# Kernel tuning notes

Hardware: AMD Instinct MI355X
Metric: run time of the kernel (lower is better)

## Reference

```python
import jax, jax.numpy as jnp
import numpy as np

D_MODEL = 1024
H = 16
D_K = D_MODEL // H


def setup_inputs() -> dict:
    key = jax.random.key(0)
    ks = jax.random.split(key, 8)
    B, S = 4, 2048
    q = jax.random.normal(ks[0], (B, S, D_MODEL), dtype=jnp.float32)
    k = jax.random.normal(ks[1], (B, S, D_MODEL), dtype=jnp.float32)
    v = jax.random.normal(ks[2], (B, S, D_MODEL), dtype=jnp.float32)
    scale = 1.0 / np.sqrt(D_MODEL)
    W_q = jax.random.normal(ks[3], (H, D_MODEL, D_K), dtype=jnp.float32) * scale
    W_k = jax.random.normal(ks[4], (H, D_MODEL, D_K), dtype=jnp.float32) * scale
    W_v = jax.random.normal(ks[5], (H, D_MODEL, D_K), dtype=jnp.float32) * scale
    W_o = jax.random.normal(ks[6], (D_MODEL, H * D_K), dtype=jnp.float32) * scale
    b_o = jax.random.normal(ks[7], (D_MODEL,), dtype=jnp.float32) * 0.01
    return {"q": q, "k": k, "v": v, "W_q": W_q, "W_k": W_k, "W_v": W_v, "W_o": W_o, "b_o": b_o}


def reference(q, k, v, W_q, W_k, W_v, W_o, b_o):
    # Per-head projections: [B,S,D] x [H,D,dk] -> [H,B,S,dk]
    qh = jnp.einsum('bsd,hdk->hbsk', q, W_q)
    kh = jnp.einsum('bsd,hdk->hbsk', k, W_k)
    vh = jnp.einsum('bsd,hdk->hbsk', v, W_v)
    # Scaled dot-product attention (full score matrix, as in original)
    scores = jnp.einsum('hbsk,hbtk->hbst', qh, kh) / jnp.sqrt(jnp.asarray(D_K, qh.dtype))
    attn = jax.nn.softmax(scores, axis=-1)
    out = jnp.einsum('hbst,hbtk->hbsk', attn, vh)  # [H,B,S,dk]
    # torch.cat(chunks along head dim, dim=2): head-major feature concat -> [B,S,H*dk]
    out = jnp.transpose(out, (1, 2, 0, 3)).reshape(q.shape[0], q.shape[1], H * D_K)
    return out @ W_o.T + b_o
```

## Files before the change

kernel.cpp:

```cpp
#include <hip/hip_runtime.h>

#define S_LEN 2048

typedef __attribute__((ext_vector_type(8))) short v8s;
typedef __attribute__((ext_vector_type(4))) short v4s;
typedef __attribute__((ext_vector_type(4))) float f32x4;
typedef __attribute__((ext_vector_type(4))) unsigned short v4us;
typedef __attribute__((ext_vector_type(4))) unsigned int v4u;

static __device__ __forceinline__ unsigned short f2bf(float x){
  unsigned u = __builtin_bit_cast(unsigned, x);
  u = (u + 0x7fffu + ((u >> 16) & 1u)) >> 16;
  return (unsigned short)u;
}

static __device__ __forceinline__ unsigned pk2(float a, float b){
  unsigned ua = __builtin_bit_cast(unsigned, a) + 0x8000u;
  unsigned ub = __builtin_bit_cast(unsigned, b) + 0x8000u;
  return __builtin_amdgcn_perm(ub, ua, 0x07060302u);
}

static __device__ __forceinline__ void gload16(const void* g, void* l){
  __builtin_amdgcn_global_load_lds((const __attribute__((address_space(1))) void*)g,
                                   (__attribute__((address_space(3))) void*)l, 16, 0, 0);
}

static __device__ __forceinline__ unsigned lds_off(const void* p){
  return (unsigned)(unsigned long long)(__attribute__((address_space(3))) const void*)p;
}

__global__ void conv_w(const float* __restrict__ Wq, const float* __restrict__ Wk,
                       const float* __restrict__ Wv, const float* __restrict__ Wo,
                       unsigned short* __restrict__ outW){
  int i = blockIdx.x*256 + threadIdx.x;
  const int stride = gridDim.x*256;
  for(; i < 4*1048576; i += stride){
    if (i < 3*1048576){
      int which = i >> 20;
      int rem = i & 1048575;
      const float* W = which==0 ? Wq : (which==1 ? Wk : Wv);
      float v = W[rem];
      if (which == 0) v *= 0.18033688011112042f;
      int h = rem >> 16, d = (rem >> 6) & 1023, kk = rem & 63;
      outW[(which<<20) + (((h<<6)+kk)<<10) + d] = f2bf(v);
    } else {
      outW[i] = f2bf(Wo[i - 3*1048576]);
    }
  }
}

__global__ __launch_bounds__(256,2) void gemm_proj(
    const float* __restrict__ Aq, const float* __restrict__ Ak, const float* __restrict__ Avv,
    const unsigned short* __restrict__ Wtb,
    unsigned short* __restrict__ C0, unsigned short* __restrict__ C1, unsigned short* __restrict__ C2){
  __shared__ unsigned short Als[128*64];
  __shared__ unsigned short Bls[128*64];
  const int tid = threadIdx.x;
  const int l = tid & 63, w = tid >> 6;
  const int z = blockIdx.z;
  const float* Af = (z==0) ? Aq : ((z==1) ? Ak : Avv);
  unsigned short* Cb = (z==0) ? C0 : ((z==1) ? C1 : C2);
  int lid = blockIdx.y*8 + blockIdx.x;
  int nid = (lid & 7)*64 + (lid >> 3);
  const int tx = nid & 7, ty = nid >> 3;
  const int m0 = ty*128, n0 = tx*128;
  const int wr = w >> 1, wc = w & 1;

  f32x4 zero = {0.f,0.f,0.f,0.f};
  f32x4 acc[4][4];
  #pragma unroll
  for(int i=0;i<4;i++){
    #pragma unroll
    for(int j=0;j<4;j++) acc[i][j] = zero;
  }

  const int xorm = (l&7)<<4;
  const int g8 = (l>>4)<<3;
  const int rsub = l>>3, csub = l&7;
  const float* Abase = Af + m0*1024;
  const unsigned short* Bbase = Wtb + z*1048576 + n0*1024;

  float4 ar[8];
  #pragma unroll
  for(int i=0;i<4;i++){
    int c = w*4+i, r = c*8+rsub;
    const float4* src = (const float4*)(Abase + r*1024 + csub*8);
    ar[2*i] = src[0]; ar[2*i+1] = src[1];
  }

  for(int kt=0; kt<16; ++kt){
    const int k0 = kt*64;
    #pragma unroll
    for(int i=0;i<4;i++){
      int c = w*4+i, r = c*8+rsub;
      v4u o = { pk2(ar[2*i].x, ar[2*i].y), pk2(ar[2*i].z, ar[2*i].w),
                pk2(ar[2*i+1].x, ar[2*i+1].y), pk2(ar[2*i+1].z, ar[2*i+1].w) };
      *(v4u*)&Als[c*512 + rsub*64 + ((csub ^ (r&7))<<3)] = o;
    }
    #pragma unroll
    for(int i=0;i<4;i++){
      int c = w*4+i, r = c*8+rsub, col = csub ^ (r&7);
      gload16(Bbase + r*1024 + k0 + col*8, (void*)&Bls[c*512]);
    }
    if (kt < 15){
      #pragma unroll
      for(int i=0;i<4;i++){
        int c = w*4+i, r = c*8+rsub;
        const float4* src = (const float4*)(Abase + r*1024 + (k0+64) + csub*8);
        ar[2*i] = src[0]; ar[2*i+1] = src[1];
      }
    }
    __syncthreads();
    const char* Ab = (const char*)Als;
    const char* Bb = (const char*)Bls;
    #pragma unroll
    for(int kk=0; kk<2; ++kk){
      v8s af[4], bfr[4];
      #pragma unroll
      for(int mf=0; mf<4; ++mf){
        int rb = (wr*64 + mf*16 + (l&15))*128;
        v4s lo = *(const v4s*)(Ab + rb + ((kk*64 + g8) ^ xorm));
        v4s hi = *(const v4s*)(Ab + rb + ((kk*64 + 32 + g8) ^ xorm));
        af[mf] = __builtin_shufflevector(lo, hi, 0,1,2,3,4,5,6,7);
      }
      #pragma unroll
      for(int nf=0; nf<4; ++nf){
        int rb = (wc*64 + nf*16 + (l&15))*128;
        v4s lo = *(const v4s*)(Bb + rb + ((kk*64 + g8) ^ xorm));
        v4s hi = *(const v4s*)(Bb + rb + ((kk*64 + 32 + g8) ^ xorm));
        bfr[nf] = __builtin_shufflevector(lo, hi, 0,1,2,3,4,5,6,7);
      }
      #pragma unroll
      for(int mf=0; mf<4; ++mf){
        #pragma unroll
        for(int nf=0; nf<4; ++nf)
          acc[mf][nf] = __builtin_amdgcn_mfma_f32_16x16x32_bf16(af[mf], bfr[nf], acc[mf][nf], 0,0,0);
      }
    }
    __syncthreads();
  }

  const int g4 = (l>>4)<<2;
  #pragma unroll
  for(int mf=0; mf<4; ++mf){
    int rowb = m0 + wr*64 + mf*16 + g4;
    #pragma unroll
    for(int nf=0; nf<4; ++nf){
      int col = n0 + wc*64 + nf*16 + (l&15);
      #pragma unroll
      for(int r=0;r<4;++r)
        Cb[(rowb+r)*1024 + col] = f2bf(acc[mf][nf][r]);
    }
  }
}

template<int EPI>
__global__ __launch_bounds__(256,2) void gemm_bt(const unsigned short* __restrict__ A,
                                                 const unsigned short* __restrict__ Bt,
                                                 void* __restrict__ Cout,
                                                 const float* __restrict__ bias){
  __shared__ unsigned short Als[128*64];
  __shared__ unsigned short Bls[128*64];
  const int tid = threadIdx.x;
  const int l = tid & 63, w = tid >> 6;
  int lid = blockIdx.y*8 + blockIdx.x;
  int nid = (lid & 7)*64 + (lid >> 3);
  const int tx = nid & 7, ty = nid >> 3;
  const int m0 = ty*128, n0 = tx*128;
  const int wr = w >> 1, wc = w & 1;

  f32x4 zero = {0.f,0.f,0.f,0.f};
  f32x4 acc[4][4];
  #pragma unroll
  for(int i=0;i<4;i++){
    #pragma unroll
    for(int j=0;j<4;j++) acc[i][j] = zero;
  }

  const int xorm = (l&7)<<4;
  const int g8 = (l>>4)<<3;
  const int rsub = l>>3, csub = l&7;
  const unsigned short* Abase = A + m0*1024;
  const unsigned short* Bbase = Bt + n0*1024;

  for(int kt=0; kt<16; ++kt){
    const int k0 = kt*64;
    #pragma unroll
    for(int i=0;i<4;i++){
      int c = w*4+i, r = c*8+rsub, col = csub ^ (r&7);
      gload16(Abase + r*1024 + k0 + col*8, (void*)&Als[c*512]);
    }
    #pragma unroll
    for(int i=0;i<4;i++){
      int c = w*4+i, r = c*8+rsub, col = csub ^ (r&7);
      gload16(Bbase + r*1024 + k0 + col*8, (void*)&Bls[c*512]);
    }
    __syncthreads();
    const char* Ab = (const char*)Als;
    const char* Bb = (const char*)Bls;
    #pragma unroll
    for(int kk=0; kk<2; ++kk){
      v8s af[4], bfr[4];
      #pragma unroll
      for(int mf=0; mf<4; ++mf){
        int rb = (wr*64 + mf*16 + (l&15))*128;
        v4s lo = *(const v4s*)(Ab + rb + ((kk*64 + g8) ^ xorm));
        v4s hi = *(const v4s*)(Ab + rb + ((kk*64 + 32 + g8) ^ xorm));
        af[mf] = __builtin_shufflevector(lo, hi, 0,1,2,3,4,5,6,7);
      }
      #pragma unroll
      for(int nf=0; nf<4; ++nf){
        int rb = (wc*64 + nf*16 + (l&15))*128;
        v4s lo = *(const v4s*)(Bb + rb + ((kk*64 + g8) ^ xorm));
        v4s hi = *(const v4s*)(Bb + rb + ((kk*64 + 32 + g8) ^ xorm));
        bfr[nf] = __builtin_shufflevector(lo, hi, 0,1,2,3,4,5,6,7);
      }
      #pragma unroll
      for(int mf=0; mf<4; ++mf){
        #pragma unroll
        for(int nf=0; nf<4; ++nf)
          acc[mf][nf] = __builtin_amdgcn_mfma_f32_16x16x32_bf16(af[mf], bfr[nf], acc[mf][nf], 0,0,0);
      }
    }
    __syncthreads();
  }

  const int g4 = (l>>4)<<2;
  if (EPI == 0){
    unsigned short* C = (unsigned short*)Cout;
    #pragma unroll
    for(int mf=0; mf<4; ++mf){
      int rowb = m0 + wr*64 + mf*16 + g4;
      #pragma unroll
      for(int nf=0; nf<4; ++nf){
        int col = n0 + wc*64 + nf*16 + (l&15);
        #pragma unroll
        for(int r=0;r<4;++r)
          C[(rowb+r)*1024 + col] = f2bf(acc[mf][nf][r]);
      }
    }
  } else {
    float* C = (float*)Cout;
    #pragma unroll
    for(int mf=0; mf<4; ++mf){
      int rowb = m0 + wr*64 + mf*16 + g4;
      #pragma unroll
      for(int nf=0; nf<4; ++nf){
        int col = n0 + wc*64 + nf*16 + (l&15);
        float bv = bias[col];
        #pragma unroll
        for(int r=0;r<4;++r)
          C[(rowb+r)*1024 + col] = acc[mf][nf][r] + bv;
      }
    }
  }
}

__global__ __launch_bounds__(256,2) void attn_fwd(const unsigned short* __restrict__ Q,
                                                  const unsigned short* __restrict__ K,
                                                  const unsigned short* __restrict__ V,
                                                  unsigned short* __restrict__ O){
  __shared__ unsigned short KVls[2][2][64*64];
  const int tid = threadIdx.x;
  const int l = tid & 63, w = tid >> 6;
  int lid = blockIdx.y*16 + blockIdx.x;
  int nid = (lid & 7)*128 + (lid >> 3);
  const int qb = nid & 15, bh = nid >> 4;
  const int b = bh >> 4, h = bh & 15;
  const int base = b*S_LEN*1024 + h*64;
  const int q0 = qb*128;
  const int xorm = (l&7)<<4, g8 = (l>>4)<<3, g4 = (l>>4)<<2;
  const int rsub = l>>3, csub = l&7;

  auto stage_kv = [&](int kt2, int buf){
    const int k0 = kt2*64;
    #pragma unroll
    for(int i=0;i<2;i++){
      int c = w*2+i, r = c*8+rsub, col = csub ^ (r&7);
      gload16(K + base + (k0+r)*1024 + col*8, (void*)&KVls[buf][0][c*512]);
    }
    #pragma unroll
    for(int i=0;i<2;i++){
      int c = w*2+i;
      int e0 = c*512 + l*8;
      int kg = e0>>10, dg = (e0>>8)&3, kin = (e0>>4)&15, din = e0&15;
      gload16(V + base + (k0 + kg*16 + kin)*1024 + dg*16 + din, (void*)&KVls[buf][1][c*512]);
    }
  };

  #pragma unroll
  for(int i=0;i<4;i++){
    int c = w*4+i, r = c*8+rsub, col = csub ^ (r&7);
    gload16(Q + base + (q0+r)*1024 + col*8, (void*)&KVls[1][0][c*512]);
  }
  stage_kv(0, 0);
  __syncthreads();

  v8s qf[2][2];
  {
    const char* Qb = (const char*)&KVls[1][0][0];
    #pragma unroll
    for(int qh=0; qh<2; ++qh){
      int rb = (w*32 + qh*16 + (l&15))*128;
      #pragma unroll
      for(int t=0;t<2;t++){
        v4s lo = *(const v4s*)(Qb + rb + ((t*64 + g8) ^ xorm));
        v4s hi = *(const v4s*)(Qb + rb + ((t*64 + 32 + g8) ^ xorm));
        qf[qh][t] = __builtin_shufflevector(lo, hi, 0,1,2,3,4,5,6,7);
      }
    }
  }
  __builtin_amdgcn_sched_barrier(0);
  __syncthreads();

  f32x4 zero = {0.f,0.f,0.f,0.f};
  f32x4 oacc[2][4];
  #pragma unroll
  for(int qh=0;qh<2;qh++){
    #pragma unroll
    for(int nf=0;nf<4;nf++) oacc[qh][nf] = zero;
  }
  float lsum[2] = {0.f, 0.f};
  const unsigned vbase0 = lds_off(&KVls[0][1][0]) + l*8;
  const unsigned vbase1 = lds_off(&KVls[1][1][0]) + l*8;

  int cur = 0;
  for(int kt=0; kt<32; ++kt){
    if (kt < 31) stage_kv(kt+1, cur^1);

    const char* Kb = (const char*)&KVls[cur][0][0];
    f32x4 sf[2][4];
    #pragma unroll
    for(int mf=0;mf<4;mf++){
      int rb = (mf*16 + (l&15))*128;
      v8s kf[2];
      #pragma unroll
      for(int t=0;t<2;t++){
        v4s lo = *(const v4s*)(Kb + rb + ((t*64 + g8) ^ xorm));
        v4s hi = *(const v4s*)(Kb + rb + ((t*64 + 32 + g8) ^ xorm));
        kf[t] = __builtin_shufflevector(lo, hi, 0,1,2,3,4,5,6,7);
      }
      #pragma unroll
      for(int qh=0;qh<2;qh++){
        sf[qh][mf] = __builtin_amdgcn_mfma_f32_16x16x32_bf16(kf[0], qf[qh][0], zero, 0,0,0);
        sf[qh][mf] = __builtin_amdgcn_mfma_f32_16x16x32_bf16(kf[1], qf[qh][1], sf[qh][mf], 0,0,0);
      }
    }

    const unsigned vb_sel = cur ? vbase1 : vbase0;
    v4s vtr[2][2][4];
    #define TRR(T,H,N,OFF) asm volatile("ds_read_b64_tr_b16 %0, %1 offset:" #OFF \
                     : "=v"(vtr[T][H][N]) : "v"(vb_sel) : "memory")
    TRR(0,0,0,0);    TRR(0,0,1,512);  TRR(0,0,2,1024); TRR(0,0,3,1536);
    TRR(0,1,0,2048); TRR(0,1,1,2560); TRR(0,1,2,3072); TRR(0,1,3,3584);
    TRR(1,0,0,4096); TRR(1,0,1,4608); TRR(1,0,2,5120); TRR(1,0,3,5632);
    TRR(1,1,0,6144); TRR(1,1,1,6656); TRR(1,1,2,7168); TRR(1,1,3,7680);
    #undef TRR

    v8s pa[2][2];
    #pragma unroll
    for(int qh=0;qh<2;qh++){
      unsigned pd[2][4];
      float ls = 0.f;
      #pragma unroll
      for(int mf=0;mf<4;mf++){
        float e0 = __builtin_amdgcn_exp2f(sf[qh][mf][0]);
        float e1 = __builtin_amdgcn_exp2f(sf[qh][mf][1]);
        float e2 = __builtin_amdgcn_exp2f(sf[qh][mf][2]);
        float e3 = __builtin_amdgcn_exp2f(sf[qh][mf][3]);
        ls += (e0+e1)+(e2+e3);
        int t = mf>>1, hf = mf&1;
        pd[t][hf*2+0] = pk2(e0, e1);
        pd[t][hf*2+1] = pk2(e2, e3);
      }
      lsum[qh] += ls;
      #pragma unroll
      for(int t=0;t<2;t++){
        v4u u = { pd[t][0], pd[t][1], pd[t][2], pd[t][3] };
        pa[qh][t] = __builtin_bit_cast(v8s, u);
      }
    }

    asm volatile("s_waitcnt lgkmcnt(0)" ::: "memory");
    __builtin_amdgcn_sched_barrier(0);
    __builtin_amdgcn_s_setprio(1);
    #pragma unroll
    for(int t=0;t<2;t++){
      #pragma unroll
      for(int nf=0;nf<4;nf++){
        v8s vb = __builtin_shufflevector(vtr[t][0][nf], vtr[t][1][nf], 0,1,2,3,4,5,6,7);
        #pragma unroll
        for(int qh=0;qh<2;qh++)
          oacc[qh][nf] = __builtin_amdgcn_mfma_f32_16x16x32_bf16(pa[qh][t], vb, oacc[qh][nf], 0,0,0);
      }
    }
    __builtin_amdgcn_s_setprio(0);
    __syncthreads();
    cur ^= 1;
  }

  #pragma unroll
  for(int qh=0;qh<2;qh++){
    float s = lsum[qh];
    s += __shfl_xor(s, 16, 64);
    s += __shfl_xor(s, 32, 64);
    float i0 = 1.f/__shfl(s, g4+0, 64);
    float i1 = 1.f/__shfl(s, g4+1, 64);
    float i2 = 1.f/__shfl(s, g4+2, 64);
    float i3 = 1.f/__shfl(s, g4+3, 64);
    const int row = q0 + w*32 + qh*16 + g4;
    #pragma unroll
    for(int nf=0;nf<4;nf++){
      int col = nf*16 + (l&15);
      O[base + (row+0)*1024 + col] = f2bf(oacc[qh][nf][0]*i0);
      O[base + (row+1)*1024 + col] = f2bf(oacc[qh][nf][1]*i1);
      O[base + (row+2)*1024 + col] = f2bf(oacc[qh][nf][2]*i2);
      O[base + (row+3)*1024 + col] = f2bf(oacc[qh][nf][3]*i3);
    }
  }
}

extern "C" void kernel_launch(void* const* d_in, const int* in_sizes, int n_in,
                              void* d_out, int out_size, void* d_ws, size_t ws_size,
                              hipStream_t stream) {
  (void)in_sizes; (void)n_in; (void)out_size;
  const float* q  = (const float*)d_in[0];
  const float* k  = (const float*)d_in[1];
  const float* v  = (const float*)d_in[2];
  const float* Wq = (const float*)d_in[3];
  const float* Wk = (const float*)d_in[4];
  const float* Wv = (const float*)d_in[5];
  const float* Wo = (const float*)d_in[6];
  const float* bo = (const float*)d_in[7];

  if (ws_size < (size_t)37748736*2) return;
  unsigned short* ws  = (unsigned short*)d_ws;
  unsigned short* Qh  = ws;
  unsigned short* Kh  = ws +  8388608;
  unsigned short* Vh  = ws + 16777216;
  unsigned short* AO  = ws + 25165824;
  unsigned short* Wt  = ws + 33554432;
  unsigned short* Wob = Wt + 3145728;

  conv_w<<<dim3(2048), dim3(256), 0, stream>>>(Wq, Wk, Wv, Wo, Wt);

  gemm_proj<<<dim3(8,64,3), dim3(256), 0, stream>>>(q, k, v, Wt, Qh, Kh, Vh);

  attn_fwd<<<dim3(16,64), dim3(256), 0, stream>>>(Qh, Kh, Vh, AO);

  gemm_bt<1><<<dim3(8,64), dim3(256), 0, stream>>>(AO, Wob, d_out, bo);
}
```

Before: 228.4 us.

## Double-buffer LDS tiles in projection and output GEMMs to overlap loads with MFMA

Both GEMM kernels now use two LDS buffers for the A and B tiles. The next k-tile is issued with global_load_lds (and, for the projection, the next fp32 A tile is converted and stored) into the alternate buffer while MFMAs run on the current one. This removes one __syncthreads per iteration and aims to hide global-load latency behind compute. LDS use doubles to 64KB per block, which may limit residency under launch_bounds(256,2). The hipcc compiler's implicit vmcnt wait before the barrier may also serialize the async loads.

```diff
diff --git a/kernel.cpp b/kernel.cpp
--- a/kernel.cpp
+++ b/kernel.cpp
@@ -53,8 +53,8 @@
     const float* __restrict__ Aq, const float* __restrict__ Ak, const float* __restrict__ Avv,
     const unsigned short* __restrict__ Wtb,
     unsigned short* __restrict__ C0, unsigned short* __restrict__ C1, unsigned short* __restrict__ C2){
-  __shared__ unsigned short Als[128*64];
-  __shared__ unsigned short Bls[128*64];
+  __shared__ unsigned short Als[2][128*64];
+  __shared__ unsigned short Bls[2][128*64];
   const int tid = threadIdx.x;
   const int l = tid & 63, w = tid >> 6;
   const int z = blockIdx.z;
@@ -87,32 +87,38 @@
     const float4* src = (const float4*)(Abase + r*1024 + csub*8);
     ar[2*i] = src[0]; ar[2*i+1] = src[1];
   }
-
+  #pragma unroll
+  for(int i=0;i<4;i++){
+    int c = w*4+i, r = c*8+rsub;
+    v4u o = { pk2(ar[2*i].x, ar[2*i].y), pk2(ar[2*i].z, ar[2*i].w),
+              pk2(ar[2*i+1].x, ar[2*i+1].y), pk2(ar[2*i+1].z, ar[2*i+1].w) };
+    *(v4u*)&Als[0][c*512 + rsub*64 + ((csub ^ (r&7))<<3)] = o;
+  }
+  #pragma unroll
+  for(int i=0;i<4;i++){
+    int c = w*4+i, r = c*8+rsub, col = csub ^ (r&7);
+    gload16(Bbase + r*1024 + col*8, (void*)&Bls[0][c*512]);
+  }
+  __syncthreads();
+
+  int cur = 0;
   for(int kt=0; kt<16; ++kt){
-    const int k0 = kt*64;
-    #pragma unroll
-    for(int i=0;i<4;i++){
-      int c = w*4+i, r = c*8+rsub;
-      v4u o = { pk2(ar[2*i].x, ar[2*i].y), pk2(ar[2*i].z, ar[2*i].w),
-                pk2(ar[2*i+1].x, ar[2*i+1].y), pk2(ar[2*i+1].z, ar[2*i+1].w) };
-      *(v4u*)&Als[c*512 + rsub*64 + ((csub ^ (r&7))<<3)] = o;
-    }
-    #pragma unroll
-    for(int i=0;i<4;i++){
-      int c = w*4+i, r = c*8+rsub, col = csub ^ (r&7);
-      gload16(Bbase + r*1024 + k0 + col*8, (void*)&Bls[c*512]);
-    }
     if (kt < 15){
+      const int k1 = (kt+1)*64;
       #pragma unroll
       for(int i=0;i<4;i++){
         int c = w*4+i, r = c*8+rsub;
-        const float4* src = (const float4*)(Abase + r*1024 + (k0+64) + csub*8);
+        const float4* src = (const float4*)(Abase + r*1024 + k1 + csub*8);
         ar[2*i] = src[0]; ar[2*i+1] = src[1];
       }
-    }
-    __syncthreads();
-    const char* Ab = (const char*)Als;
-    const char* Bb = (const char*)Bls;
+      #pragma unroll
+      for(int i=0;i<4;i++){
+        int c = w*4+i, r = c*8+rsub, col = csub ^ (r&7);
+        gload16(Bbase + r*1024 + k1 + col*8, (void*)&Bls[cur^1][c*512]);
+      }
+    }
+    const char* Ab = (const char*)&Als[cur][0];
+    const char* Bb = (const char*)&Bls[cur][0];
     #pragma unroll
     for(int kk=0; kk<2; ++kk){
       v8s af[4], bfr[4];
@@ -137,7 +143,17 @@
           acc[mf][nf] = __builtin_amdgcn_mfma_f32_16x16x32_bf16(af[mf], bfr[nf], acc[mf][nf], 0,0,0);
       }
     }
+    if (kt < 15){
+      #pragma unroll
+      for(int i=0;i<4;i++){
+        int c = w*4+i, r = c*8+rsub;
+        v4u o = { pk2(ar[2*i].x, ar[2*i].y), pk2(ar[2*i].z, ar[2*i].w),
+                  pk2(ar[2*i+1].x, ar[2*i+1].y), pk2(ar[2*i+1].z, ar[2*i+1].w) };
+        *(v4u*)&Als[cur^1][c*512 + rsub*64 + ((csub ^ (r&7))<<3)] = o;
+      }
+    }
     __syncthreads();
+    cur ^= 1;
   }
 
   const int g4 = (l>>4)<<2;
@@ -159,8 +175,8 @@
                                                  const unsigned short* __restrict__ Bt,
                                                  void* __restrict__ Cout,
                                                  const float* __restrict__ bias){
-  __shared__ unsigned short Als[128*64];
-  __shared__ unsigned short Bls[128*64];
+  __shared__ unsigned short Als[2][128*64];
+  __shared__ unsigned short Bls[2][128*64];
   const int tid = threadIdx.x;
   const int l = tid & 63, w = tid >> 6;
   int lid = blockIdx.y*8 + blockIdx.x;
@@ -183,21 +199,35 @@
   const unsigned short* Abase = A + m0*1024;
   const unsigned short* Bbase = Bt + n0*1024;
 
+  #pragma unroll
+  for(int i=0;i<4;i++){
+    int c = w*4+i, r = c*8+rsub, col = csub ^ (r&7);
+    gload16(Abase + r*1024 + col*8, (void*)&Als[0][c*512]);
+  }
+  #pragma unroll
+  for(int i=0;i<4;i++){
+    int c = w*4+i, r = c*8+rsub, col = csub ^ (r&7);
+    gload16(Bbase + r*1024 + col*8, (void*)&Bls[0][c*512]);
+  }
+  __syncthreads();
+
+  int cur = 0;
   for(int kt=0; kt<16; ++kt){
-    const int k0 = kt*64;
-    #pragma unroll
-    for(int i=0;i<4;i++){
-      int c = w*4+i, r = c*8+rsub, col = csub ^ (r&7);
-      gload16(Abase + r*1024 + k0 + col*8, (void*)&Als[c*512]);
-    }
-    #pragma unroll
-    for(int i=0;i<4;i++){
-      int c = w*4+i, r = c*8+rsub, col = csub ^ (r&7);
-      gload16(Bbase + r*1024 + k0 + col*8, (void*)&Bls[c*512]);
-    }
-    __syncthreads();
-    const char* Ab = (const char*)Als;
-    const char* Bb = (const char*)Bls;
+    if (kt < 15){
+      const int k1 = (kt+1)*64;
+      #pragma unroll
+      for(int i=0;i<4;i++){
+        int c = w*4+i, r = c*8+rsub, col = csub ^ (r&7);
+        gload16(Abase + r*1024 + k1 + col*8, (void*)&Als[cur^1][c*512]);
+      }
+      #pragma unroll
+      for(int i=0;i<4;i++){
+        int c = w*4+i, r = c*8+rsub, col = csub ^ (r&7);
+        gload16(Bbase + r*1024 + k1 + col*8, (void*)&Bls[cur^1][c*512]);
+      }
+    }
+    const char* Ab = (const char*)&Als[cur][0];
+    const char* Bb = (const char*)&Bls[cur][0];
     #pragma unroll
     for(int kk=0; kk<2; ++kk){
       v8s af[4], bfr[4];
@@ -223,6 +253,7 @@
       }
     }
     __syncthreads();
+    cur ^= 1;
   }
 
   const int g4 = (l>>4)<<2;
```

Result: slower. 234.1 us (+2.5%).
